# Performance work log

Hardware: AMD Instinct MI355X
Metric: run time of the kernel (lower is better)

## Reference

```python
import jax, jax.numpy as jnp
import numpy as np

N, F = 8000, 256
NEG_SLOPE = 0.2


def setup_inputs() -> dict:
    key = jax.random.key(0)
    k1, k2, k3, k4, k5, k6, k7 = jax.random.split(key, 7)
    node_embeddings = jax.random.normal(k1, (N, F), dtype=jnp.float32)
    adj_matrix = jax.random.randint(k2, (N, N), 0, 2, dtype=jnp.int32)
    # Learned params: W (Linear F->F with bias), a (Linear 2F->1 with bias).
    # a's weight [1, 2F] is split into a_src (first F, applied to H_i) and
    # a_dst (last F, applied to H_j) -- mathematically identical to the
    # concat-then-linear formulation, without the N*N*2F intermediate.
    s = 1.0 / np.sqrt(F)
    W_w = jax.random.uniform(k3, (F, F), dtype=jnp.float32, minval=-s, maxval=s)
    W_b = jax.random.uniform(k4, (F,), dtype=jnp.float32, minval=-s, maxval=s)
    s2 = 1.0 / np.sqrt(2 * F)
    a_src = jax.random.uniform(k5, (F,), dtype=jnp.float32, minval=-s2, maxval=s2)
    a_dst = jax.random.uniform(k6, (F,), dtype=jnp.float32, minval=-s2, maxval=s2)
    a_b = jax.random.uniform(k7, (), dtype=jnp.float32, minval=-s2, maxval=s2)
    return {
        "node_embeddings": node_embeddings,
        "adj_matrix": adj_matrix,
        "W_w": W_w,
        "W_b": W_b,
        "a_src": a_src,
        "a_dst": a_dst,
        "a_b": a_b,
    }


def reference(node_embeddings, adj_matrix, W_w, W_b, a_src, a_dst, a_b):
    # H = W(x)
    H = node_embeddings @ W_w.T + W_b                      # [N, F]
    # e_ij = a([H_i ; H_j]) = H_i . a_src + H_j . a_dst + b
    e = (H @ a_src)[:, None] + (H @ a_dst)[None, :] + a_b  # [N, N]
    # mask BEFORE leakyrelu (as in the original), then leakyrelu, then softmax
    e = jnp.where(adj_matrix == 0, -jnp.inf, e)
    e = jnp.where(e >= 0, e, NEG_SLOPE * e)                # leakyrelu(-inf) = -inf
    attn = jax.nn.softmax(e, axis=1)                       # [N, N]
    return attn @ H                                        # [N, F]
```

## Files before the change

kernel.cpp:

```cpp
#include <hip/hip_runtime.h>

#define NN 8000
#define FD 256
#define NEG_SLOPE 0.2f
#define BM 64
#define KT 32
#define JS 4
#define CHUNK 2016

typedef __bf16 bf16;
typedef __bf16 bf16x8 __attribute__((ext_vector_type(8)));
typedef __bf16 bf16x4 __attribute__((ext_vector_type(4)));
typedef float f32x4 __attribute__((ext_vector_type(4)));

__global__ __launch_bounds__(256) void k_linear(const float* __restrict__ X,
                                                const float* __restrict__ W,
                                                const float* __restrict__ b,
                                                bf16* __restrict__ Ht,
                                                float* __restrict__ out,
                                                float* __restrict__ lg) {
    __shared__ float Xs[16][260];
    const int t = threadIdx.x;
    const int i0 = blockIdx.x * 16;
    {
        const int gt = blockIdx.x * 256 + t;
        const float4 z4 = {0.f, 0.f, 0.f, 0.f};
        float4* o4 = (float4*)out;
        #pragma unroll
        for (int k = 0; k < 4; ++k) o4[gt + k * 128000] = z4;
        if (gt < NN) lg[gt] = 0.f;
    }
    #pragma unroll
    for (int r = 0; r < 16; ++r)
        Xs[r][t] = X[(size_t)(i0 + r) * FD + t];
    __syncthreads();
    const int f = t;
    float acc[16];
    const float bf_ = b[f];
    #pragma unroll
    for (int ii = 0; ii < 16; ++ii) acc[ii] = bf_;
    for (int k4 = 0; k4 < FD / 4; ++k4) {
        const float4 w4 = *(const float4*)&W[(size_t)f * FD + k4 * 4];
        #pragma unroll
        for (int ii = 0; ii < 16; ++ii) {
            const float4 x4 = *(const float4*)&Xs[ii][k4 * 4];
            acc[ii] += x4.x * w4.x + x4.y * w4.y + x4.z * w4.z + x4.w * w4.w;
        }
    }
    bf16x8 v0, v1;
    #pragma unroll
    for (int ii = 0; ii < 8; ++ii) { v0[ii] = (bf16)acc[ii]; v1[ii] = (bf16)acc[ii + 8]; }
    *(bf16x8*)&Ht[(size_t)f * NN + i0]     = v0;
    *(bf16x8*)&Ht[(size_t)f * NN + i0 + 8] = v1;
}

__global__ __launch_bounds__(256) void k_attn_vec(const bf16* __restrict__ Ht,
                                                  const float* __restrict__ a_src,
                                                  const float* __restrict__ a_dst,
                                                  const float* __restrict__ a_b,
                                                  float* __restrict__ hs,
                                                  float* __restrict__ hd) {
    __shared__ float psh[4][64], pdh[4][64];
    const int t = threadIdx.x;
    const int li = t & 63;
    const int q = t >> 6;
    const int i = blockIdx.x * 64 + li;
    float ps = 0.f, pd = 0.f;
    #pragma unroll 8
    for (int fi = 0; fi < 64; ++fi) {
        const int f = q * 64 + fi;
        const float h = (float)Ht[(size_t)f * NN + i];
        ps += h * a_src[f];
        pd += h * a_dst[f];
    }
    psh[q][li] = ps; pdh[q][li] = pd;
    __syncthreads();
    if (q == 0) {
        ps = psh[0][li] + psh[1][li] + psh[2][li] + psh[3][li];
        pd = pdh[0][li] + pdh[1][li] + pdh[2][li] + pdh[3][li];
        hs[i] = ps + a_b[0];
        hd[i] = pd;
    }
}

__global__ __launch_bounds__(512, 4) void k_gat(const bf16* __restrict__ Ht,
                                                const int* __restrict__ adj,
                                                const float* __restrict__ hs,
                                                const float* __restrict__ hd,
                                                float* __restrict__ out,
                                                float* __restrict__ lg) {
    __shared__ __attribute__((aligned(16))) bf16 Bt[2][FD * KT];
    __shared__ __attribute__((aligned(16))) bf16 Wt[2][BM * KT];

    const int t  = threadIdx.x;
    const int l  = t & 63;
    const int wv = t >> 6;
    const int ib = blockIdx.x >> 2;
    const int jb = blockIdx.x & 3;
    const int i0 = ib * BM;
    const int jq0 = jb * CHUNK;
    const int NS = (jb < 3) ? 63 : 61;

    const int r  = t >> 3;
    const int jm = (t & 7) << 2;
    const float hsv = hs[i0 + r];
    const int* adjp  = adj + (size_t)(i0 + r) * NN + jq0 + jm;
    const float* hdp = hd + jq0 + jm;
    const int woff = r * 64 + (((jm >> 3) ^ ((r >> 2) & 3)) << 4) + (((jm >> 2) & 1) << 3);

    const int al = l & 15, asl = l >> 4;
    const int eff = (asl ^ ((al >> 2) & 3)) << 4;

    auto stage = [&](int s_, int bufi) {
        #pragma unroll
        for (int q = 0; q < 2; ++q) {
            const int idx = q * 512 + t;
            const int col = idx >> 2;
            const int kk = (idx & 3) ^ ((col >> 2) & 3);
            const bf16* src = Ht + (size_t)col * NN + jq0 + s_ * KT + kk * 8;
            bf16* dst = &Bt[bufi][(q * 512 + wv * 64) * 8];
            __builtin_amdgcn_global_load_lds(
                (const __attribute__((address_space(1))) void*)src,
                (__attribute__((address_space(3))) void*)dst, 16, 0, 0);
        }
    };

    int4   adjc = *(const int4*)adjp;
    float4 hdc  = *(const float4*)hdp;
    stage(0, 0);

    f32x4 acc[4][2];
    #pragma unroll
    for (int sr = 0; sr < 4; ++sr) {
        acc[sr][0] = (f32x4){0.f, 0.f, 0.f, 0.f};
        acc[sr][1] = (f32x4){0.f, 0.f, 0.f, 0.f};
    }
    float lsum = 0.f;

    #pragma unroll 1
    for (int s = 0; s < NS; ++s) {
        const int cur = s & 1;
        int4 adjn; float4 hdn;
        if (s + 1 < NS) {
            adjn = *(const int4*)(adjp + (size_t)(s + 1) * KT);
            hdn  = *(const float4*)(hdp + (size_t)(s + 1) * KT);
            stage(s + 1, cur ^ 1);
        }

        {
            float e, w0, w1, w2, w3;
            e = hsv + hdc.x; e = e >= 0.f ? e : NEG_SLOPE * e; w0 = adjc.x ? __expf(e) : 0.f;
            e = hsv + hdc.y; e = e >= 0.f ? e : NEG_SLOPE * e; w1 = adjc.y ? __expf(e) : 0.f;
            e = hsv + hdc.z; e = e >= 0.f ? e : NEG_SLOPE * e; w2 = adjc.z ? __expf(e) : 0.f;
            e = hsv + hdc.w; e = e >= 0.f ? e : NEG_SLOPE * e; w3 = adjc.w ? __expf(e) : 0.f;
            lsum += (w0 + w1) + (w2 + w3);
            bf16x4 wp; wp[0] = (bf16)w0; wp[1] = (bf16)w1; wp[2] = (bf16)w2; wp[3] = (bf16)w3;
            *(bf16x4*)((char*)&Wt[cur][0] + woff) = wp;
        }

        if (s + 1 < NS) asm volatile("s_waitcnt vmcnt(4)" ::: "memory");
        else            asm volatile("s_waitcnt vmcnt(0)" ::: "memory");
        asm volatile("s_waitcnt lgkmcnt(0)" ::: "memory");
        __builtin_amdgcn_s_barrier();

        {
            const char* wb = (const char*)&Wt[cur][0];
            const char* bb = (const char*)&Bt[cur][0];
            bf16x8 a[4], b[2];
            #pragma unroll
            for (int sr = 0; sr < 4; ++sr)
                a[sr] = *(const bf16x8*)(wb + (sr * 16 + al) * 64 + eff);
            #pragma unroll
            for (int cf = 0; cf < 2; ++cf)
                b[cf] = *(const bf16x8*)(bb + (wv * 32 + cf * 16 + al) * 64 + eff);
            #pragma unroll
            for (int sr = 0; sr < 4; ++sr) {
                acc[sr][0] = __builtin_amdgcn_mfma_f32_16x16x32_bf16(a[sr], b[0], acc[sr][0], 0, 0, 0);
                acc[sr][1] = __builtin_amdgcn_mfma_f32_16x16x32_bf16(a[sr], b[1], acc[sr][1], 0, 0, 0);
            }
        }
        asm volatile("s_waitcnt lgkmcnt(0)" ::: "memory");
        __builtin_amdgcn_s_barrier();

        adjc = adjn; hdc = hdn;
    }

    lsum += __shfl_xor(lsum, 1);
    lsum += __shfl_xor(lsum, 2);
    lsum += __shfl_xor(lsum, 4);
    if ((t & 7) == 0) atomicAdd(&lg[i0 + r], lsum);

    #pragma unroll
    for (int sr = 0; sr < 4; ++sr) {
        #pragma unroll
        for (int cf = 0; cf < 2; ++cf) {
            #pragma unroll
            for (int g = 0; g < 4; ++g) {
                atomicAdd(&out[(size_t)(i0 + sr * 16 + asl * 4 + g) * FD + wv * 32 + cf * 16 + al],
                          acc[sr][cf][g]);
            }
        }
    }
}

__global__ __launch_bounds__(256) void k_norm(float* __restrict__ out,
                                              const float* __restrict__ lg) {
    const int i = blockIdx.x;
    const float rinv = 1.0f / lg[i];
    out[(size_t)i * FD + threadIdx.x] *= rinv;
}

extern "C" void kernel_launch(void* const* d_in, const int* in_sizes, int n_in,
                              void* d_out, int out_size, void* d_ws, size_t ws_size,
                              hipStream_t stream) {
    const float* X     = (const float*)d_in[0];
    const int*   adj   = (const int*)d_in[1];
    const float* Ww    = (const float*)d_in[2];
    const float* Wb    = (const float*)d_in[3];
    const float* a_src = (const float*)d_in[4];
    const float* a_dst = (const float*)d_in[5];
    const float* a_b   = (const float*)d_in[6];
    float* out = (float*)d_out;

    bf16*  Ht = (bf16*)d_ws;
    float* hs = (float*)((char*)d_ws + (size_t)FD * NN * sizeof(bf16));
    float* hd = hs + NN;
    float* lg = hd + NN;

    k_linear<<<NN / 16, 256, 0, stream>>>(X, Ww, Wb, Ht, out, lg);
    k_attn_vec<<<NN / 64, 256, 0, stream>>>(Ht, a_src, a_dst, a_b, hs, hd);
    k_gat<<<(NN / BM) * JS, 512, 0, stream>>>(Ht, adj, hs, hd, out, lg);
    k_norm<<<NN, 256, 0, stream>>>(out, lg);
}
```

Measured before the change: 150.9 us.

## Stage adjacency through LDS with async loads and retile GAT wave layout

```diff
diff --git a/kernel.cpp b/kernel.cpp
--- a/kernel.cpp
+++ b/kernel.cpp
@@ -5,8 +5,7 @@
 #define NEG_SLOPE 0.2f
 #define BM 64
 #define KT 32
-#define JS 4
-#define CHUNK 2016
+#define JCH 2048
 
 typedef __bf16 bf16;
 typedef __bf16 bf16x8 __attribute__((ext_vector_type(8)));
@@ -83,106 +82,118 @@
     }
 }
 
-__global__ __launch_bounds__(512, 4) void k_gat(const bf16* __restrict__ Ht,
+__global__ __launch_bounds__(512, 2) void k_gat(const bf16* __restrict__ Ht,
                                                 const int* __restrict__ adj,
                                                 const float* __restrict__ hs,
                                                 const float* __restrict__ hd,
                                                 float* __restrict__ out,
                                                 float* __restrict__ lg) {
     __shared__ __attribute__((aligned(16))) bf16 Bt[2][FD * KT];
-    __shared__ __attribute__((aligned(16))) bf16 Wt[2][BM * KT];
+    __shared__ __attribute__((aligned(16))) int  Adt[3][BM * KT];
+    __shared__ __attribute__((aligned(16))) bf16 Wt[2][BM * 40];
+    __shared__ float hd_s[JCH];
 
     const int t  = threadIdx.x;
     const int l  = t & 63;
     const int wv = t >> 6;
+    const int jb = blockIdx.x & 3;
     const int ib = blockIdx.x >> 2;
-    const int jb = blockIdx.x & 3;
     const int i0 = ib * BM;
-    const int jq0 = jb * CHUNK;
-    const int NS = (jb < 3) ? 63 : 61;
+    const int j0 = jb * JCH;
+    const int NS = (jb < 3) ? 64 : 58;
 
     const int r  = t >> 3;
-    const int jm = (t & 7) << 2;
+    const int js = t & 7;
     const float hsv = hs[i0 + r];
-    const int* adjp  = adj + (size_t)(i0 + r) * NN + jq0 + jm;
-    const float* hdp = hd + jq0 + jm;
-    const int woff = r * 64 + (((jm >> 3) ^ ((r >> 2) & 3)) << 4) + (((jm >> 2) & 1) << 3);
-
+
+    const int is = wv >> 2, fg = wv & 3;
     const int al = l & 15, asl = l >> 4;
-    const int eff = (asl ^ ((al >> 2) & 3)) << 4;
-
-    auto stage = [&](int s_, int bufi) {
+    const int bswz = (asl ^ ((al >> 2) & 3)) << 4;
+
+    auto stage_bt = [&](int s_, int buf) {
         #pragma unroll
         for (int q = 0; q < 2; ++q) {
             const int idx = q * 512 + t;
-            const int col = idx >> 2;
-            const int kk = (idx & 3) ^ ((col >> 2) & 3);
-            const bf16* src = Ht + (size_t)col * NN + jq0 + s_ * KT + kk * 8;
-            bf16* dst = &Bt[bufi][(q * 512 + wv * 64) * 8];
+            const int col = idx >> 2, ks = idx & 3;
+            const bf16* src = Ht + (size_t)col * NN + j0 + s_ * KT
+                              + ((ks ^ ((col >> 2) & 3)) * 8);
+            bf16* dst = &Bt[buf][idx * 8];
             __builtin_amdgcn_global_load_lds(
                 (const __attribute__((address_space(1))) void*)src,
                 (__attribute__((address_space(3))) void*)dst, 16, 0, 0);
         }
     };
-
-    int4   adjc = *(const int4*)adjp;
-    float4 hdc  = *(const float4*)hdp;
-    stage(0, 0);
-
-    f32x4 acc[4][2];
-    #pragma unroll
-    for (int sr = 0; sr < 4; ++sr) {
-        acc[sr][0] = (f32x4){0.f, 0.f, 0.f, 0.f};
-        acc[sr][1] = (f32x4){0.f, 0.f, 0.f, 0.f};
-    }
+    auto stage_ad = [&](int s_, int buf) {
+        const int* src = adj + (size_t)(i0 + r) * NN + j0 + s_ * KT + js * 4;
+        int* dst = &Adt[buf][t * 4];
+        __builtin_amdgcn_global_load_lds(
+            (const __attribute__((address_space(1))) void*)src,
+            (__attribute__((address_space(3))) void*)dst, 16, 0, 0);
+    };
+
+    stage_ad(0, 0);
+    stage_ad(1, 1);
+    stage_bt(0, 0);
+    {
+        const int jg = j0 + t * 4;
+        float4 h4 = {0.f, 0.f, 0.f, 0.f};
+        if (jg + 3 < NN) h4 = *(const float4*)(hd + jg);
+        *(float4*)&hd_s[t * 4] = h4;
+    }
+    asm volatile("s_waitcnt lgkmcnt(0)" ::: "memory");
+    __builtin_amdgcn_s_barrier();
+
+    f32x4 acc[2][4];
+    #pragma unroll
+    for (int rb = 0; rb < 2; ++rb)
+        #pragma unroll
+        for (int cf = 0; cf < 4; ++cf) acc[rb][cf] = (f32x4){0.f, 0.f, 0.f, 0.f};
     float lsum = 0.f;
 
     #pragma unroll 1
     for (int s = 0; s < NS; ++s) {
-        const int cur = s & 1;
-        int4 adjn; float4 hdn;
-        if (s + 1 < NS) {
-            adjn = *(const int4*)(adjp + (size_t)(s + 1) * KT);
-            hdn  = *(const float4*)(hdp + (size_t)(s + 1) * KT);
-            stage(s + 1, cur ^ 1);
-        }
+        const int bt = s & 1;
+        if (s + 1 < NS) stage_bt(s + 1, (s + 1) & 1);
+        if (s + 2 < NS) stage_ad(s + 2, (s + 2) % 3);
+        if (s + 2 < NS)      asm volatile("s_waitcnt vmcnt(3)" ::: "memory");
+        else if (s + 1 < NS) asm volatile("s_waitcnt vmcnt(2)" ::: "memory");
+        else                 asm volatile("s_waitcnt vmcnt(0)" ::: "memory");
 
         {
+            const int4 a4 = *(const int4*)&Adt[s % 3][t * 4];
+            const float4 h4 = *(const float4*)&hd_s[s * KT + js * 4];
             float e, w0, w1, w2, w3;
-            e = hsv + hdc.x; e = e >= 0.f ? e : NEG_SLOPE * e; w0 = adjc.x ? __expf(e) : 0.f;
-            e = hsv + hdc.y; e = e >= 0.f ? e : NEG_SLOPE * e; w1 = adjc.y ? __expf(e) : 0.f;
-            e = hsv + hdc.z; e = e >= 0.f ? e : NEG_SLOPE * e; w2 = adjc.z ? __expf(e) : 0.f;
-            e = hsv + hdc.w; e = e >= 0.f ? e : NEG_SLOPE * e; w3 = adjc.w ? __expf(e) : 0.f;
+            e = hsv + h4.x; e = fmaxf(e, NEG_SLOPE * e); w0 = a4.x ? __expf(e) : 0.f;
+            e = hsv + h4.y; e = fmaxf(e, NEG_SLOPE * e); w1 = a4.y ? __expf(e) : 0.f;
+            e = hsv + h4.z; e = fmaxf(e, NEG_SLOPE * e); w2 = a4.z ? __expf(e) : 0.f;
+            e = hsv + h4.w; e = fmaxf(e, NEG_SLOPE * e); w3 = a4.w ? __expf(e) : 0.f;
             lsum += (w0 + w1) + (w2 + w3);
-            bf16x4 wp; wp[0] = (bf16)w0; wp[1] = (bf16)w1; wp[2] = (bf16)w2; wp[3] = (bf16)w3;
-            *(bf16x4*)((char*)&Wt[cur][0] + woff) = wp;
-        }
-
-        if (s + 1 < NS) asm volatile("s_waitcnt vmcnt(4)" ::: "memory");
-        else            asm volatile("s_waitcnt vmcnt(0)" ::: "memory");
+            bf16x4 w4v;
+            w4v[0] = (bf16)w0; w4v[1] = (bf16)w1; w4v[2] = (bf16)w2; w4v[3] = (bf16)w3;
+            *(bf16x4*)((char*)&Wt[bt][0] + r * 80 + js * 8) = w4v;
+        }
         asm volatile("s_waitcnt lgkmcnt(0)" ::: "memory");
         __builtin_amdgcn_s_barrier();
 
         {
-            const char* wb = (const char*)&Wt[cur][0];
-            const char* bb = (const char*)&Bt[cur][0];
-            bf16x8 a[4], b[2];
-            #pragma unroll
-            for (int sr = 0; sr < 4; ++sr)
-                a[sr] = *(const bf16x8*)(wb + (sr * 16 + al) * 64 + eff);
-            #pragma unroll
-            for (int cf = 0; cf < 2; ++cf)
-                b[cf] = *(const bf16x8*)(bb + (wv * 32 + cf * 16 + al) * 64 + eff);
-            #pragma unroll
-            for (int sr = 0; sr < 4; ++sr) {
-                acc[sr][0] = __builtin_amdgcn_mfma_f32_16x16x32_bf16(a[sr], b[0], acc[sr][0], 0, 0, 0);
-                acc[sr][1] = __builtin_amdgcn_mfma_f32_16x16x32_bf16(a[sr], b[1], acc[sr][1], 0, 0, 0);
-            }
+            const char* Ab = (const char*)&Wt[bt][0];
+            const char* Bb = (const char*)&Bt[bt][0];
+            bf16x8 a[2], b[4];
+            #pragma unroll
+            for (int rb = 0; rb < 2; ++rb)
+                a[rb] = *(const bf16x8*)(Ab + (is * 32 + rb * 16 + al) * 80 + asl * 16);
+            #pragma unroll
+            for (int cf = 0; cf < 4; ++cf)
+                b[cf] = *(const bf16x8*)(Bb + (fg * 64 + cf * 16 + al) * 64 + bswz);
+            #pragma unroll
+            for (int rb = 0; rb < 2; ++rb)
+                #pragma unroll
+                for (int cf = 0; cf < 4; ++cf)
+                    acc[rb][cf] = __builtin_amdgcn_mfma_f32_16x16x32_bf16(
+                        a[rb], b[cf], acc[rb][cf], 0, 0, 0);
         }
         asm volatile("s_waitcnt lgkmcnt(0)" ::: "memory");
         __builtin_amdgcn_s_barrier();
-
-        adjc = adjn; hdc = hdn;
     }
 
     lsum += __shfl_xor(lsum, 1);
@@ -191,16 +202,13 @@
     if ((t & 7) == 0) atomicAdd(&lg[i0 + r], lsum);
 
     #pragma unroll
-    for (int sr = 0; sr < 4; ++sr) {
-        #pragma unroll
-        for (int cf = 0; cf < 2; ++cf) {
-            #pragma unroll
-            for (int g = 0; g < 4; ++g) {
-                atomicAdd(&out[(size_t)(i0 + sr * 16 + asl * 4 + g) * FD + wv * 32 + cf * 16 + al],
-                          acc[sr][cf][g]);
-            }
-        }
-    }
+    for (int rb = 0; rb < 2; ++rb)
+        #pragma unroll
+        for (int cf = 0; cf < 4; ++cf)
+            #pragma unroll
+            for (int g = 0; g < 4; ++g)
+                atomicAdd(&out[(size_t)(i0 + is * 32 + rb * 16 + asl * 4 + g) * FD
+                               + fg * 64 + cf * 16 + al], acc[rb][cf][g]);
 }
 
 __global__ __launch_bounds__(256) void k_norm(float* __restrict__ out,
@@ -229,6 +237,6 @@
 
     k_linear<<<NN / 16, 256, 0, stream>>>(X, Ww, Wb, Ht, out, lg);
     k_attn_vec<<<NN / 64, 256, 0, stream>>>(Ht, a_src, a_dst, a_b, hs, hd);
-    k_gat<<<(NN / BM) * JS, 512, 0, stream>>>(Ht, adj, hs, hd, out, lg);
+    k_gat<<<125 * 4, 512, 0, stream>>>(Ht, adj, hs, hd, out, lg);
     k_norm<<<NN, 256, 0, stream>>>(out, lg);
 }
```

After: 150.5 us. About the same (-0.3%).

## Enlarge GAT row tile, split j into 8 partials, drop atomics

Applied to the files above, without the earlier changes.

```diff
diff --git a/kernel.cpp b/kernel.cpp
--- a/kernel.cpp
+++ b/kernel.cpp
@@ -3,33 +3,24 @@
 #define NN 8000
 #define FD 256
 #define NEG_SLOPE 0.2f
-#define BM 64
+#define BM 128
 #define KT 32
-#define JS 4
-#define CHUNK 2016
+#define NJB 8
+#define JCH 1024
 
 typedef __bf16 bf16;
 typedef __bf16 bf16x8 __attribute__((ext_vector_type(8)));
-typedef __bf16 bf16x4 __attribute__((ext_vector_type(4)));
 typedef float f32x4 __attribute__((ext_vector_type(4)));
+
+#define MFMA16 __builtin_amdgcn_mfma_f32_16x16x32_bf16
 
 __global__ __launch_bounds__(256) void k_linear(const float* __restrict__ X,
                                                 const float* __restrict__ W,
                                                 const float* __restrict__ b,
-                                                bf16* __restrict__ Ht,
-                                                float* __restrict__ out,
-                                                float* __restrict__ lg) {
+                                                bf16* __restrict__ Ht) {
     __shared__ float Xs[16][260];
     const int t = threadIdx.x;
     const int i0 = blockIdx.x * 16;
-    {
-        const int gt = blockIdx.x * 256 + t;
-        const float4 z4 = {0.f, 0.f, 0.f, 0.f};
-        float4* o4 = (float4*)out;
-        #pragma unroll
-        for (int k = 0; k < 4; ++k) o4[gt + k * 128000] = z4;
-        if (gt < NN) lg[gt] = 0.f;
-    }
     #pragma unroll
     for (int r = 0; r < 16; ++r)
         Xs[r][t] = X[(size_t)(i0 + r) * FD + t];
@@ -87,127 +78,155 @@
                                                 const int* __restrict__ adj,
                                                 const float* __restrict__ hs,
                                                 const float* __restrict__ hd,
-                                                float* __restrict__ out,
-                                                float* __restrict__ lg) {
+                                                float* __restrict__ outP,
+                                                float* __restrict__ lgP) {
     __shared__ __attribute__((aligned(16))) bf16 Bt[2][FD * KT];
-    __shared__ __attribute__((aligned(16))) bf16 Wt[2][BM * KT];
+    __shared__ __attribute__((aligned(16))) int  Adt[2][BM * KT];
+    __shared__ __attribute__((aligned(16))) char Wt[BM * 72];
+    __shared__ float hd_s[JCH];
 
     const int t  = threadIdx.x;
     const int l  = t & 63;
     const int wv = t >> 6;
-    const int ib = blockIdx.x >> 2;
-    const int jb = blockIdx.x & 3;
+    const int jb = blockIdx.x & 7;
+    const int ib = blockIdx.x >> 3;
     const int i0 = ib * BM;
-    const int jq0 = jb * CHUNK;
-    const int NS = (jb < 3) ? 63 : 61;
-
-    const int r  = t >> 3;
-    const int jm = (t & 7) << 2;
-    const float hsv = hs[i0 + r];
-    const int* adjp  = adj + (size_t)(i0 + r) * NN + jq0 + jm;
-    const float* hdp = hd + jq0 + jm;
-    const int woff = r * 64 + (((jm >> 3) ^ ((r >> 2) & 3)) << 4) + (((jm >> 2) & 1) << 3);
+    const int j0 = jb * JCH;
+    const int NS = (jb < 7) ? 32 : 26;
+
+    const int r   = t >> 2;
+    const int js4 = t & 3;
+    const int ig  = min(i0 + r, NN - 1);
+    const float hsv = hs[ig];
 
     const int al = l & 15, asl = l >> 4;
-    const int eff = (asl ^ ((al >> 2) & 3)) << 4;
-
-    auto stage = [&](int s_, int bufi) {
+    const int wr = wv >> 2, wc = wv & 3;
+
+    auto stage_ad = [&](int s_, int buf) {
+        const int* src = adj + (size_t)ig * NN + j0 + s_ * KT + js4 * 8;
+        __builtin_amdgcn_global_load_lds(
+            (const __attribute__((address_space(1))) void*)src,
+            (__attribute__((address_space(3))) void*)&Adt[buf][t * 4], 16, 0, 0);
+        __builtin_amdgcn_global_load_lds(
+            (const __attribute__((address_space(1))) void*)(src + 4),
+            (__attribute__((address_space(3))) void*)&Adt[buf][2048 + t * 4], 16, 0, 0);
+    };
+    auto stage_bt = [&](int s_, int buf) {
         #pragma unroll
         for (int q = 0; q < 2; ++q) {
             const int idx = q * 512 + t;
-            const int col = idx >> 2;
-            const int kk = (idx & 3) ^ ((col >> 2) & 3);
-            const bf16* src = Ht + (size_t)col * NN + jq0 + s_ * KT + kk * 8;
-            bf16* dst = &Bt[bufi][(q * 512 + wv * 64) * 8];
+            const int f = idx >> 2, sl = idx & 3;
+            const int ss = sl ^ ((f >> 2) & 3);
+            const bf16* src = Ht + (size_t)f * NN + j0 + s_ * KT + ss * 8;
             __builtin_amdgcn_global_load_lds(
                 (const __attribute__((address_space(1))) void*)src,
-                (__attribute__((address_space(3))) void*)dst, 16, 0, 0);
+                (__attribute__((address_space(3))) void*)&Bt[buf][idx * 8], 16, 0, 0);
         }
     };
 
-    int4   adjc = *(const int4*)adjp;
-    float4 hdc  = *(const float4*)hdp;
-    stage(0, 0);
-
-    f32x4 acc[4][2];
-    #pragma unroll
-    for (int sr = 0; sr < 4; ++sr) {
-        acc[sr][0] = (f32x4){0.f, 0.f, 0.f, 0.f};
-        acc[sr][1] = (f32x4){0.f, 0.f, 0.f, 0.f};
-    }
+    {
+        const int jg = j0 + t * 2;
+        float2 h2 = {0.f, 0.f};
+        if (jg + 1 < NN) h2 = *(const float2*)(hd + jg);
+        *(float2*)&hd_s[t * 2] = h2;
+    }
+    asm volatile("s_waitcnt vmcnt(0) lgkmcnt(0)" ::: "memory");
+    stage_ad(0, 0);
+    stage_bt(0, 0);
+    __builtin_amdgcn_s_barrier();
+
+    f32x4 acc[4][4];
+    #pragma unroll
+    for (int rb = 0; rb < 4; ++rb)
+        #pragma unroll
+        for (int cf = 0; cf < 4; ++cf) acc[rb][cf] = (f32x4){0.f, 0.f, 0.f, 0.f};
     float lsum = 0.f;
 
     #pragma unroll 1
     for (int s = 0; s < NS; ++s) {
-        const int cur = s & 1;
-        int4 adjn; float4 hdn;
-        if (s + 1 < NS) {
-            adjn = *(const int4*)(adjp + (size_t)(s + 1) * KT);
-            hdn  = *(const float4*)(hdp + (size_t)(s + 1) * KT);
-            stage(s + 1, cur ^ 1);
-        }
-
-        {
-            float e, w0, w1, w2, w3;
-            e = hsv + hdc.x; e = e >= 0.f ? e : NEG_SLOPE * e; w0 = adjc.x ? __expf(e) : 0.f;
-            e = hsv + hdc.y; e = e >= 0.f ? e : NEG_SLOPE * e; w1 = adjc.y ? __expf(e) : 0.f;
-            e = hsv + hdc.z; e = e >= 0.f ? e : NEG_SLOPE * e; w2 = adjc.z ? __expf(e) : 0.f;
-            e = hsv + hdc.w; e = e >= 0.f ? e : NEG_SLOPE * e; w3 = adjc.w ? __expf(e) : 0.f;
-            lsum += (w0 + w1) + (w2 + w3);
-            bf16x4 wp; wp[0] = (bf16)w0; wp[1] = (bf16)w1; wp[2] = (bf16)w2; wp[3] = (bf16)w3;
-            *(bf16x4*)((char*)&Wt[cur][0] + woff) = wp;
-        }
-
+        const int buf = s & 1;
+        if (s + 1 < NS) { stage_ad(s + 1, buf ^ 1); stage_bt(s + 1, buf ^ 1); }
         if (s + 1 < NS) asm volatile("s_waitcnt vmcnt(4)" ::: "memory");
         else            asm volatile("s_waitcnt vmcnt(0)" ::: "memory");
+
+        {
+            const int4 alo = *(const int4*)&Adt[buf][t * 4];
+            const int4 ahi = *(const int4*)&Adt[buf][2048 + t * 4];
+            const float4 hlo = *(const float4*)&hd_s[s * KT + js4 * 8];
+            const float4 hhi = *(const float4*)&hd_s[s * KT + js4 * 8 + 4];
+            float e, w0, w1, w2, w3, w4, w5, w6, w7;
+            e = hsv + hlo.x; e = fmaxf(e, NEG_SLOPE * e); w0 = alo.x ? __expf(e) : 0.f;
+            e = hsv + hlo.y; e = fmaxf(e, NEG_SLOPE * e); w1 = alo.y ? __expf(e) : 0.f;
+            e = hsv + hlo.z; e = fmaxf(e, NEG_SLOPE * e); w2 = alo.z ? __expf(e) : 0.f;
+            e = hsv + hlo.w; e = fmaxf(e, NEG_SLOPE * e); w3 = alo.w ? __expf(e) : 0.f;
+            e = hsv + hhi.x; e = fmaxf(e, NEG_SLOPE * e); w4 = ahi.x ? __expf(e) : 0.f;
+            e = hsv + hhi.y; e = fmaxf(e, NEG_SLOPE * e); w5 = ahi.y ? __expf(e) : 0.f;
+            e = hsv + hhi.z; e = fmaxf(e, NEG_SLOPE * e); w6 = ahi.z ? __expf(e) : 0.f;
+            e = hsv + hhi.w; e = fmaxf(e, NEG_SLOPE * e); w7 = ahi.w ? __expf(e) : 0.f;
+            lsum += ((w0 + w1) + (w2 + w3)) + ((w4 + w5) + (w6 + w7));
+            bf16x8 w8;
+            w8[0] = (bf16)w0; w8[1] = (bf16)w1; w8[2] = (bf16)w2; w8[3] = (bf16)w3;
+            w8[4] = (bf16)w4; w8[5] = (bf16)w5; w8[6] = (bf16)w6; w8[7] = (bf16)w7;
+            *(bf16x8*)(Wt + r * 72 + js4 * 16) = w8;
+        }
         asm volatile("s_waitcnt lgkmcnt(0)" ::: "memory");
         __builtin_amdgcn_s_barrier();
 
         {
-            const char* wb = (const char*)&Wt[cur][0];
-            const char* bb = (const char*)&Bt[cur][0];
-            bf16x8 a[4], b[2];
+            bf16x8 b[4];
             #pragma unroll
-            for (int sr = 0; sr < 4; ++sr)
-                a[sr] = *(const bf16x8*)(wb + (sr * 16 + al) * 64 + eff);
+            for (int cf = 0; cf < 4; ++cf) {
+                const int f = wc * 64 + cf * 16 + al;
+                b[cf] = *(const bf16x8*)((const char*)&Bt[buf][0] + f * 64
+                                         + ((asl ^ ((f >> 2) & 3)) << 4));
+            }
             #pragma unroll
-            for (int cf = 0; cf < 2; ++cf)
-                b[cf] = *(const bf16x8*)(bb + (wv * 32 + cf * 16 + al) * 64 + eff);
-            #pragma unroll
-            for (int sr = 0; sr < 4; ++sr) {
-                acc[sr][0] = __builtin_amdgcn_mfma_f32_16x16x32_bf16(a[sr], b[0], acc[sr][0], 0, 0, 0);
-                acc[sr][1] = __builtin_amdgcn_mfma_f32_16x16x32_bf16(a[sr], b[1], acc[sr][1], 0, 0, 0);
+            for (int rb = 0; rb < 4; ++rb) {
+                const bf16x8 a = *(const bf16x8*)(Wt + (wr * 64 + rb * 16 + al) * 72
+                                                  + asl * 16);
+                acc[rb][0] = MFMA16(a, b[0], acc[rb][0], 0, 0, 0);
+                acc[rb][1] = MFMA16(a, b[1], acc[rb][1], 0, 0, 0);
+                acc[rb][2] = MFMA16(a, b[2], acc[rb][2], 0, 0, 0);
+                acc[rb][3] = MFMA16(a, b[3], acc[rb][3], 0, 0, 0);
             }
         }
         asm volatile("s_waitcnt lgkmcnt(0)" ::: "memory");
         __builtin_amdgcn_s_barrier();
-
-        adjc = adjn; hdc = hdn;
     }
 
     lsum += __shfl_xor(lsum, 1);
     lsum += __shfl_xor(lsum, 2);
-    lsum += __shfl_xor(lsum, 4);
-    if ((t & 7) == 0) atomicAdd(&lg[i0 + r], lsum);
-
-    #pragma unroll
-    for (int sr = 0; sr < 4; ++sr) {
-        #pragma unroll
-        for (int cf = 0; cf < 2; ++cf) {
-            #pragma unroll
-            for (int g = 0; g < 4; ++g) {
-                atomicAdd(&out[(size_t)(i0 + sr * 16 + asl * 4 + g) * FD + wv * 32 + cf * 16 + al],
-                          acc[sr][cf][g]);
+    if (js4 == 0 && i0 + r < NN) lgP[(size_t)jb * NN + i0 + r] = lsum;
+
+    float* op = outP + (size_t)jb * NN * FD;
+    #pragma unroll
+    for (int rb = 0; rb < 4; ++rb) {
+        #pragma unroll
+        for (int g = 0; g < 4; ++g) {
+            const int i = i0 + wr * 64 + rb * 16 + asl * 4 + g;
+            if (i < NN) {
+                float* orow = op + (size_t)i * FD + wc * 64 + al;
+                orow[0]  = acc[rb][0][g];
+                orow[16] = acc[rb][1][g];
+                orow[32] = acc[rb][2][g];
+                orow[48] = acc[rb][3][g];
             }
         }
     }
 }
 
-__global__ __launch_bounds__(256) void k_norm(float* __restrict__ out,
-                                              const float* __restrict__ lg) {
+__global__ __launch_bounds__(256) void k_norm(const float* __restrict__ outP,
+                                              const float* __restrict__ lgP,
+                                              float* __restrict__ out) {
     const int i = blockIdx.x;
-    const float rinv = 1.0f / lg[i];
-    out[(size_t)i * FD + threadIdx.x] *= rinv;
+    const int f = threadIdx.x;
+    float ls = 0.f;
+    #pragma unroll
+    for (int c = 0; c < NJB; ++c) ls += lgP[(size_t)c * NN + i];
+    float v = 0.f;
+    #pragma unroll
+    for (int c = 0; c < NJB; ++c) v += outP[(size_t)c * NN * FD + (size_t)i * FD + f];
+    out[(size_t)i * FD + f] = v * (1.0f / ls);
 }
 
 extern "C" void kernel_launch(void* const* d_in, const int* in_sizes, int n_in,
@@ -222,13 +241,14 @@
     const float* a_b   = (const float*)d_in[6];
     float* out = (float*)d_out;
 
-    bf16*  Ht = (bf16*)d_ws;
-    float* hs = (float*)((char*)d_ws + (size_t)FD * NN * sizeof(bf16));
-    float* hd = hs + NN;
-    float* lg = hd + NN;
-
-    k_linear<<<NN / 16, 256, 0, stream>>>(X, Ww, Wb, Ht, out, lg);
+    bf16*  Ht   = (bf16*)d_ws;
+    float* hs   = (float*)((char*)d_ws + (size_t)FD * NN * sizeof(bf16));
+    float* hd   = hs + NN;
+    float* lgP  = hd + NN;
+    float* outP = lgP + (size_t)NJB * NN;
+
+    k_linear<<<NN / 16, 256, 0, stream>>>(X, Ww, Wb, Ht);
     k_attn_vec<<<NN / 64, 256, 0, stream>>>(Ht, a_src, a_dst, a_b, hs, hd);
-    k_gat<<<(NN / BM) * JS, 512, 0, stream>>>(Ht, adj, hs, hd, out, lg);
-    k_norm<<<NN, 256, 0, stream>>>(out, lg);
-}
+    k_gat<<<63 * NJB, 512, 0, stream>>>(Ht, adj, hs, hd, outP, lgP);
+    k_norm<<<NN, 256, 0, stream>>>(outP, lgP, out);
+}
```

Measured after the change: 151.4 us. No clear change (+0.3%).
